# Performance work log

Measured on AMD Instinct MI355X. Metric: run time of the kernel, lower is better.

Reference implementation:

```python
import jax, jax.numpy as jnp
import numpy as np

DT = 0.01
NJ = 7
GRAV = 9.81
Q_LOWER = jnp.array([-2.9671, -1.8326, -2.9671, -3.1416, -2.9671, -0.0873, -2.9671], jnp.float32)
Q_UPPER = jnp.array([ 2.9671,  1.8326,  2.9671,  0.0,     2.9671,  3.8223,  2.9671], jnp.float32)


def _skew(v):
    z = jnp.zeros((), v.dtype)
    return jnp.stack([jnp.stack([z, -v[2], v[1]]),
                      jnp.stack([v[2], z, -v[0]]),
                      jnp.stack([-v[1], v[0], z])])


def _mot_X(E, r):
    # 6x6 spatial motion transform [[E,0],[-E*skew(r),E]]
    zero = jnp.zeros_like(E)
    top = jnp.concatenate([E, zero], axis=1)
    bot = jnp.concatenate([-E @ _skew(r), E], axis=1)
    return jnp.concatenate([top, bot], axis=0)


def _crm(v):
    # spatial motion cross-product matrix for v=[w;v0]
    Sw, Sv = _skew(v[:3]), _skew(v[3:])
    zero = jnp.zeros_like(Sw)
    top = jnp.concatenate([Sw, zero], axis=1)
    bot = jnp.concatenate([Sv, Sw], axis=1)
    return jnp.concatenate([top, bot], axis=0)


def _step_single(x, u, axes, R_tree, p_tree, I_sp):
    dt_ = x.dtype
    q = jnp.clip(x[:NJ], Q_LOWER.astype(dt_), Q_UPPER.astype(dt_))
    qd = x[NJ:]
    # forward kinematics: per-joint 6x6 child<-parent transforms and motion subspaces
    Xups, Ss = [], []
    eye3 = jnp.eye(3, dtype=dt_)
    for i in range(NJ):
        a = axes[i]
        c, s = jnp.cos(q[i]), jnp.sin(q[i])
        R = c * eye3 + s * _skew(a) + (1.0 - c) * jnp.outer(a, a)  # rodrigues
        Xj = _mot_X(R.T, jnp.zeros(3, dt_))
        Xt = _mot_X(R_tree[i], p_tree[i])
        Xups.append(Xj @ Xt)
        Ss.append(jnp.concatenate([a, jnp.zeros(3, dt_)]))
    # RNEA bias force h (qdd=0, gravity, zero base velocity, identity base pose)
    v_prev = jnp.zeros(6, dt_)
    a_prev = jnp.array([0.0, 0.0, 0.0, 0.0, 0.0, GRAV], dt_)  # a_base = -g trick
    fs = []
    for i in range(NJ):
        vJ = Ss[i] * qd[i]
        v = Xups[i] @ v_prev + vJ
        acc = Xups[i] @ a_prev + _crm(v) @ vJ
        Iv = I_sp[i] @ v
        f = I_sp[i] @ acc - _crm(v).T @ Iv  # crf(v) = -crm(v)^T
        fs.append(f)
        v_prev, a_prev = v, acc
    h = [None] * NJ
    for i in range(NJ - 1, -1, -1):
        h[i] = Ss[i] @ fs[i]
        if i > 0:
            fs[i - 1] = fs[i - 1] + Xups[i].T @ fs[i]
    h = jnp.stack(h)
    # CRBA mass matrix (serial chain, parent(i)=i-1)
    Ic = [I_sp[i] for i in range(NJ)]
    M = jnp.zeros((NJ, NJ), dt_)
    for i in range(NJ - 1, -1, -1):
        if i > 0:
            Ic[i - 1] = Ic[i - 1] + Xups[i].T @ Ic[i] @ Xups[i]
        F = Ic[i] @ Ss[i]
        M = M.at[i, i].set(Ss[i] @ F)
        for j in range(i - 1, -1, -1):
            F = Xups[j + 1].T @ F
            mij = Ss[j] @ F
            M = M.at[i, j].set(mij).at[j, i].set(mij)
    M = M + 1e-8 * jnp.eye(NJ, dtype=dt_)
    qdd = jnp.linalg.solve(M, (u - h)[:, None])[:, 0]
    qd_new = qd + DT * qdd
    q_new = q + DT * qd_new
    return jnp.concatenate([q_new, qd_new])


def setup_inputs() -> dict:
    B = 65536
    key = jax.random.key(0)
    k1, k2 = jax.random.split(key)
    x = jax.random.normal(k1, (B, 14), jnp.float32)
    u = jax.random.normal(k2, (B, 7), jnp.float32)
    rng = np.random.default_rng(0)
    # unit joint axes
    axes = rng.normal(size=(NJ, 3))
    axes = axes / np.linalg.norm(axes, axis=1, keepdims=True)
    # orthonormal fixed parent->child rotations (det +1)
    R_tree = np.empty((NJ, 3, 3))
    for i in range(NJ):
        Q, _ = np.linalg.qr(rng.normal(size=(3, 3)))
        if np.linalg.det(Q) < 0:
            Q[:, 0] = -Q[:, 0]
        R_tree[i] = Q
    p_tree = 0.2 * rng.normal(size=(NJ, 3))
    # SPD 6x6 spatial inertias: [[Ibar, m*Cx],[m*Cx^T, m*I3]]
    I_sp = np.empty((NJ, 6, 6))
    for i in range(NJ):
        m = float(rng.uniform(1.0, 5.0))
        c = 0.05 * rng.normal(size=3)
        Cx = np.array([[0, -c[2], c[1]], [c[2], 0, -c[0]], [-c[1], c[0], 0]])
        A = 0.1 * rng.normal(size=(3, 3))
        Ic_ = A @ A.T + 0.05 * np.eye(3)
        Ibar = Ic_ + m * Cx @ Cx.T
        I_sp[i] = np.block([[Ibar, m * Cx], [m * Cx.T, m * np.eye(3)]])
    return {
        "x": x, "u": u,
        "axes": jnp.asarray(axes, jnp.float32),
        "R_tree": jnp.asarray(R_tree, jnp.float32),
        "p_tree": jnp.asarray(p_tree, jnp.float32),
        "I_sp": jnp.asarray(I_sp, jnp.float32),
    }


def reference(x, u, axes, R_tree, p_tree, I_sp):
    return jax.vmap(_step_single, in_axes=(0, 0, None, None, None, None))(
        x, u, axes, R_tree, p_tree, I_sp)
```

## Files before the change

kernel.cpp:

```cpp
#include <hip/hip_runtime.h>
#include <math.h>

#define NJ 7
#define DTF 0.01f
#define GRAVF 9.81f
#define MIX(i,j) ((i)*((i)+1)/2 + (j))
#define MPAD 29
#define FSTR 43
#define SNC  15
#define QST  9

__device__ __forceinline__ void cross3(const float* a, const float* b, float* o){
    o[0] = a[1]*b[2] - a[2]*b[1];
    o[1] = a[2]*b[0] - a[0]*b[2];
    o[2] = a[0]*b[1] - a[1]*b[0];
}
__device__ __forceinline__ void mv3(const float* E, const float* x, float* y){
    y[0] = E[0]*x[0] + E[1]*x[1] + E[2]*x[2];
    y[1] = E[3]*x[0] + E[4]*x[1] + E[5]*x[2];
    y[2] = E[6]*x[0] + E[7]*x[1] + E[8]*x[2];
}
__device__ __forceinline__ void mtv3(const float* E, const float* x, float* y){
    y[0] = E[0]*x[0] + E[3]*x[1] + E[6]*x[2];
    y[1] = E[1]*x[0] + E[4]*x[1] + E[7]*x[2];
    y[2] = E[2]*x[0] + E[5]*x[1] + E[8]*x[2];
}
__device__ __forceinline__ void symv(const float* S, const float* x, float* y){
    y[0] = S[0]*x[0] + S[1]*x[1] + S[2]*x[2];
    y[1] = S[1]*x[0] + S[3]*x[1] + S[4]*x[2];
    y[2] = S[2]*x[0] + S[4]*x[1] + S[5]*x[2];
}
__device__ __forceinline__ void mm3(const float* A, const float* B, float* o){
#pragma unroll
    for (int r = 0; r < 3; r++)
#pragma unroll
        for (int c = 0; c < 3; c++)
            o[r*3+c] = A[r*3]*B[c] + A[r*3+1]*B[3+c] + A[r*3+2]*B[6+c];
}
__device__ __forceinline__ void congr(const float* E, const float* X, float* o){
    float t[9];
#pragma unroll
    for (int r = 0; r < 3; r++)
#pragma unroll
        for (int c = 0; c < 3; c++)
            t[r*3+c] = E[r]*X[c] + E[3+r]*X[3+c] + E[6+r]*X[6+c];
    mm3(t, E, o);
}
__device__ __forceinline__ void makeE(const float* a, const float* __restrict__ Rt,
                                      float s, float c, float* E){
    float omc = 1.0f - c;
    float RT[9];
    RT[0] = c + omc*a[0]*a[0];       RT[1] =  s*a[2] + omc*a[0]*a[1]; RT[2] = -s*a[1] + omc*a[0]*a[2];
    RT[3] = -s*a[2] + omc*a[1]*a[0]; RT[4] = c + omc*a[1]*a[1];       RT[5] =  s*a[0] + omc*a[1]*a[2];
    RT[6] =  s*a[1] + omc*a[2]*a[0]; RT[7] = -s*a[0] + omc*a[2]*a[1]; RT[8] = c + omc*a[2]*a[2];
    float Rl[9];
#pragma unroll
    for (int k = 0; k < 9; k++) Rl[k] = Rt[k];
    mm3(RT, Rl, E);
}
__device__ __forceinline__ void bodyI(const float* __restrict__ g_I, int i,
                                      float* SA, float* h, float& m){
    const float* I6 = g_I + i*36;
    SA[0]=I6[0]; SA[1]=I6[1]; SA[2]=I6[2];
    SA[3]=I6[7]; SA[4]=I6[8]; SA[5]=I6[14];
    h[0]=I6[16]; h[1]=I6[5]; h[2]=I6[9];
    m = I6[21];
}

__constant__ float QL_c[NJ] = {-2.9671f,-1.8326f,-2.9671f,-3.1416f,-2.9671f,-0.0873f,-2.9671f};
__constant__ float QU_c[NJ] = { 2.9671f, 1.8326f, 2.9671f, 0.0f,    2.9671f, 3.8223f, 2.9671f};

__global__ __launch_bounds__(128)
void panda_step(const float* __restrict__ x, const float* __restrict__ u,
                const float* __restrict__ g_ax, const float* __restrict__ g_Rt,
                const float* __restrict__ g_pt, const float* __restrict__ g_I,
                float* __restrict__ out, int B)
{
    __shared__ float s_M[64*MPAD];
    __shared__ float s_F[2*64*FSTR];
    __shared__ float s_snc[64*SNC];
    __shared__ float s_qd[64*QST];
    __shared__ float s_rhs[64*QST];

    const int role = threadIdx.x >> 6;
    const int lane = threadIdx.x & 63;
    const int e    = blockIdx.x*64 + lane;
    const bool act = (e < B);

    float q[NJ], qd[NJ];
    if (act && role == 0){
        float xl[14];
        const float2* x2 = (const float2*)(x + e*14);
#pragma unroll
        for (int i = 0; i < 7; i++){ float2 v = x2[i]; xl[2*i] = v.x; xl[2*i+1] = v.y; }
#pragma unroll
        for (int i = 0; i < NJ; i++){
            q[i]  = fminf(fmaxf(xl[i], QL_c[i]), QU_c[i]);
            qd[i] = xl[NJ + i];
            float s, c; __sincosf(q[i], &s, &c);
            s_snc[lane*SNC + i]     = s;
            s_snc[lane*SNC + 7 + i] = c;
            s_qd[lane*QST + i]      = qd[i];
            s_rhs[lane*QST + i]     = u[e*NJ + i];
        }
    }
    __syncthreads();

    if (act && role == 1){
        float* Fb = &s_F[64*FSTR + lane*FSTR];
        float SA[6], hc[3], mc;
        bodyI(g_I, 6, SA, hc, mc);
#pragma unroll 1
        for (int i = NJ-1; i >= 0; --i){
            float a[3] = { g_ax[3*i], g_ax[3*i+1], g_ax[3*i+2] };
            float p[3] = { g_pt[3*i], g_pt[3*i+1], g_pt[3*i+2] };
            float Ft[3]; symv(SA, a, Ft);
            Fb[i*6+0]=Ft[0]; Fb[i*6+1]=Ft[1]; Fb[i*6+2]=Ft[2];
            Fb[i*6+3] = a[1]*hc[2] - a[2]*hc[1];
            Fb[i*6+4] = a[2]*hc[0] - a[0]*hc[2];
            Fb[i*6+5] = a[0]*hc[1] - a[1]*hc[0];
#pragma unroll 1
            for (int k = i; k < NJ; ++k){
                float f0=Fb[k*6], f1=Fb[k*6+1], f2=Fb[k*6+2];
                s_M[lane*MPAD + k*(k+1)/2 + i] = a[0]*f0 + a[1]*f1 + a[2]*f2;
            }
            if (i > 0){
                float snv = s_snc[lane*SNC+i], csv = s_snc[lane*SNC+7+i];
                float E[9]; makeE(a, g_Rt + 9*i, snv, csv, E);
                float SAm[6], hm[3], mm_;
                bodyI(g_I, i-1, SAm, hm, mm_);
                float Af[9] = {SA[0],SA[1],SA[2], SA[1],SA[3],SA[4], SA[2],SA[4],SA[5]};
                float Ap[9]; congr(E, Af, Ap);
                float hr[3]; mtv3(E, hc, hr);
                float hpd = hr[0]*p[0]+hr[1]*p[1]+hr[2]*p[2];
                float ppd = p[0]*p[0]+p[1]*p[1]+p[2]*p[2];
                float dga = 2.0f*hpd + mc*ppd;
                SA[0] = Ap[0] - 2.0f*p[0]*hr[0] - mc*p[0]*p[0] + dga + SAm[0];
                SA[1] = Ap[1] - p[0]*hr[1] - hr[0]*p[1] - mc*p[0]*p[1] + SAm[1];
                SA[2] = Ap[2] - p[0]*hr[2] - hr[0]*p[2] - mc*p[0]*p[2] + SAm[2];
                SA[3] = Ap[4] - 2.0f*p[1]*hr[1] - mc*p[1]*p[1] + dga + SAm[3];
                SA[4] = Ap[5] - p[1]*hr[2] - hr[1]*p[2] - mc*p[1]*p[2] + SAm[4];
                SA[5] = Ap[8] - 2.0f*p[2]*hr[2] - mc*p[2]*p[2] + dga + SAm[5];
                hc[0] = hr[0] + mc*p[0] + hm[0];
                hc[1] = hr[1] + mc*p[1] + hm[1];
                hc[2] = hr[2] + mc*p[2] + hm[2];
                mc += mm_;
#pragma unroll 1
                for (int k = i; k < NJ; ++k){
                    float ft[3] = {Fb[k*6+0], Fb[k*6+1], Fb[k*6+2]};
                    float fb[3] = {Fb[k*6+3], Fb[k*6+4], Fb[k*6+5]};
                    float tm[3], tf[3], cp[3];
                    mtv3(E, ft, tm); mtv3(E, fb, tf);
                    cross3(p, tf, cp);
                    Fb[k*6+0]=tm[0]+cp[0]; Fb[k*6+1]=tm[1]+cp[1]; Fb[k*6+2]=tm[2]+cp[2];
                    Fb[k*6+3]=tf[0];       Fb[k*6+4]=tf[1];       Fb[k*6+5]=tf[2];
                }
            }
        }
        float Mx[28];
#pragma unroll
        for (int j = 0; j < 28; j++) Mx[j] = s_M[lane*MPAD + j];
#pragma unroll
        for (int i = 0; i < NJ; i++) Mx[MIX(i,i)] += 1e-8f;
#pragma unroll
        for (int k = 0; k < NJ; k++){
            float d = Mx[MIX(k,k)];
#pragma unroll
            for (int j = 0; j < NJ; j++) if (j < k) d -= Mx[MIX(k,j)]*Mx[MIX(k,j)];
            float linv = __builtin_amdgcn_rsqf(d);
            Mx[MIX(k,k)] = linv;
#pragma unroll
            for (int i2 = k+1; i2 < NJ; i2++){
                float s2 = Mx[MIX(i2,k)];
#pragma unroll
                for (int j = 0; j < NJ; j++) if (j < k) s2 -= Mx[MIX(i2,j)]*Mx[MIX(k,j)];
                Mx[MIX(i2,k)] = s2 * linv;
            }
        }
#pragma unroll
        for (int j = 0; j < 28; j++) s_M[lane*MPAD + j] = Mx[j];
    }
    else if (act){
        float* Fb = &s_F[lane*FSTR];
        float w[3]  = {0.f,0.f,0.f}, vl[3] = {0.f,0.f,0.f};
        float aw[3] = {0.f,0.f,0.f}, av[3] = {0.f,0.f,GRAVF};
#pragma unroll 1
        for (int i = 0; i < NJ; ++i){
            float a[3] = { g_ax[3*i], g_ax[3*i+1], g_ax[3*i+2] };
            float p[3] = { g_pt[3*i], g_pt[3*i+1], g_pt[3*i+2] };
            float snv = s_snc[lane*SNC+i], csv = s_snc[lane*SNC+7+i];
            float qdi = s_qd[lane*QST+i];
            float E[9]; makeE(a, g_Rt + 9*i, snv, csv, E);
            float tw[3]; mv3(E, w, tw);
            float nw[3] = { tw[0]+a[0]*qdi, tw[1]+a[1]*qdi, tw[2]+a[2]*qdi };
            float cwp[3]; cross3(w, p, cwp);
            float t1[3] = { vl[0]+cwp[0], vl[1]+cwp[1], vl[2]+cwp[2] };
            float nvl[3]; mv3(E, t1, nvl);
            float taw[3]; mv3(E, aw, taw);
            float cna[3]; cross3(nw, a, cna);
            float naw[3] = { taw[0]+qdi*cna[0], taw[1]+qdi*cna[1], taw[2]+qdi*cna[2] };
            float cap[3]; cross3(aw, p, cap);
            float t2[3] = { av[0]+cap[0], av[1]+cap[1], av[2]+cap[2] };
            float tav[3]; mv3(E, t2, tav);
            float cva[3]; cross3(nvl, a, cva);
            float nav[3] = { tav[0]+qdi*cva[0], tav[1]+qdi*cva[1], tav[2]+qdi*cva[2] };
            float SAi[6], hi[3], mi; bodyI(g_I, i, SAi, hi, mi);
            float Ivt[3], Iat[3], hxv[3], hxa[3];
            symv(SAi, nw, Ivt);  cross3(hi, nvl, hxv);
            symv(SAi, naw, Iat); cross3(hi, nav, hxa);
#pragma unroll
            for (int k = 0; k < 3; k++){ Ivt[k] += hxv[k]; Iat[k] += hxa[k]; }
            float hxw[3], hxaw[3];
            cross3(hi, nw, hxw); cross3(hi, naw, hxaw);
            float Ivb[3] = { mi*nvl[0]-hxw[0], mi*nvl[1]-hxw[1], mi*nvl[2]-hxw[2] };
            float Iab[3] = { mi*nav[0]-hxaw[0], mi*nav[1]-hxaw[1], mi*nav[2]-hxaw[2] };
            float c1[3], c2[3], c3[3];
            cross3(nw, Ivt, c1); cross3(nvl, Ivb, c2); cross3(nw, Ivb, c3);
            Fb[i*6+0] = Iat[0]+c1[0]+c2[0];
            Fb[i*6+1] = Iat[1]+c1[1]+c2[1];
            Fb[i*6+2] = Iat[2]+c1[2]+c2[2];
            Fb[i*6+3] = Iab[0]+c3[0];
            Fb[i*6+4] = Iab[1]+c3[1];
            Fb[i*6+5] = Iab[2]+c3[2];
#pragma unroll
            for (int k = 0; k < 3; k++){ w[k]=nw[k]; vl[k]=nvl[k]; aw[k]=naw[k]; av[k]=nav[k]; }
        }
#pragma unroll 1
        for (int i = NJ-1; i >= 0; --i){
            float a[3] = { g_ax[3*i], g_ax[3*i+1], g_ax[3*i+2] };
            float f0=Fb[i*6+0], f1=Fb[i*6+1], f2=Fb[i*6+2];
            s_rhs[lane*QST+i] -= a[0]*f0 + a[1]*f1 + a[2]*f2;
            if (i > 0){
                float p[3] = { g_pt[3*i], g_pt[3*i+1], g_pt[3*i+2] };
                float snv = s_snc[lane*SNC+i], csv = s_snc[lane*SNC+7+i];
                float E[9]; makeE(a, g_Rt + 9*i, snv, csv, E);
                float ftop[3] = {f0, f1, f2};
                float fbot[3] = {Fb[i*6+3], Fb[i*6+4], Fb[i*6+5]};
                float tm[3], tf[3], cp[3];
                mtv3(E, ftop, tm); mtv3(E, fbot, tf);
                cross3(p, tf, cp);
                Fb[(i-1)*6+0] += tm[0]+cp[0];
                Fb[(i-1)*6+1] += tm[1]+cp[1];
                Fb[(i-1)*6+2] += tm[2]+cp[2];
                Fb[(i-1)*6+3] += tf[0];
                Fb[(i-1)*6+4] += tf[1];
                Fb[(i-1)*6+5] += tf[2];
            }
        }
    }

    __syncthreads();

    if (act && role == 0){
        float Mx[28];
#pragma unroll
        for (int j = 0; j < 28; j++) Mx[j] = s_M[lane*MPAD + j];
        float rhs[NJ];
#pragma unroll
        for (int i = 0; i < NJ; i++) rhs[i] = s_rhs[lane*QST + i];
        float y[NJ];
#pragma unroll
        for (int i = 0; i < NJ; i++){
            float s2 = rhs[i];
#pragma unroll
            for (int j = 0; j < NJ; j++) if (j < i) s2 -= Mx[MIX(i,j)]*y[j];
            y[i] = s2 * Mx[MIX(i,i)];
        }
        float z[NJ];
#pragma unroll
        for (int i = NJ-1; i >= 0; i--){
            float s2 = y[i];
#pragma unroll
            for (int j = NJ-1; j >= 0; j--) if (j > i) s2 -= Mx[MIX(j,i)]*z[j];
            z[i] = s2 * Mx[MIX(i,i)];
        }
        float o14[14];
#pragma unroll
        for (int i = 0; i < NJ; i++){
            float qdn = qd[i] + DTF*z[i];
            o14[i]      = q[i] + DTF*qdn;
            o14[NJ + i] = qdn;
        }
        float2* o2 = (float2*)(out + e*14);
#pragma unroll
        for (int i = 0; i < 7; i++){ float2 v; v.x = o14[2*i]; v.y = o14[2*i+1]; o2[i] = v; }
    }
}

extern "C" void kernel_launch(void* const* d_in, const int* in_sizes, int n_in,
                              void* d_out, int out_size, void* d_ws, size_t ws_size,
                              hipStream_t stream) {
    const float* x   = (const float*)d_in[0];
    const float* u   = (const float*)d_in[1];
    const float* ax  = (const float*)d_in[2];
    const float* Rt  = (const float*)d_in[3];
    const float* pt  = (const float*)d_in[4];
    const float* Isp = (const float*)d_in[5];
    float* out = (float*)d_out;
    int B = in_sizes[0] / 14;
    int grid = (B + 63) / 64;
    hipLaunchKernelGGL(panda_step, dim3(grid), dim3(128), 0, stream,
                       x, u, ax, Rt, pt, Isp, out, B);
}
```

Baseline: 77.28 us.

## Drop prologue barrier by loading inputs per role and move Cholesky to solver

Each wavefront role now loads x and computes its own sin/cos in private shared buffers, which removes the first __syncthreads and the serial prologue that only role 0 ran. The Cholesky factorization moves from the mass-matrix wavefront into the final solve section after the barrier, which shortens the longer CRBA branch. In exchange the sincos work and the x loads are done twice, once by each wavefront.

```diff
diff --git a/kernel.cpp b/kernel.cpp
--- a/kernel.cpp
+++ b/kernel.cpp
@@ -7,8 +7,8 @@
 #define MIX(i,j) ((i)*((i)+1)/2 + (j))
 #define MPAD 29
 #define FSTR 43
-#define SNC  15
-#define QST  9
+#define P0S  29
+#define P1S  15
 
 __device__ __forceinline__ void cross3(const float* a, const float* b, float* o){
     o[0] = a[1]*b[2] - a[2]*b[1];
@@ -78,9 +78,8 @@
 {
     __shared__ float s_M[64*MPAD];
     __shared__ float s_F[2*64*FSTR];
-    __shared__ float s_snc[64*SNC];
-    __shared__ float s_qd[64*QST];
-    __shared__ float s_rhs[64*QST];
+    __shared__ float s_p0[64*P0S];
+    __shared__ float s_p1[64*P1S];
 
     const int role = threadIdx.x >> 6;
     const int lane = threadIdx.x & 63;
@@ -88,25 +87,21 @@
     const bool act = (e < B);
 
     float q[NJ], qd[NJ];
-    if (act && role == 0){
-        float xl[14];
-        const float2* x2 = (const float2*)(x + e*14);
-#pragma unroll
-        for (int i = 0; i < 7; i++){ float2 v = x2[i]; xl[2*i] = v.x; xl[2*i+1] = v.y; }
-#pragma unroll
-        for (int i = 0; i < NJ; i++){
-            q[i]  = fminf(fmaxf(xl[i], QL_c[i]), QU_c[i]);
-            qd[i] = xl[NJ + i];
-            float s, c; __sincosf(q[i], &s, &c);
-            s_snc[lane*SNC + i]     = s;
-            s_snc[lane*SNC + 7 + i] = c;
-            s_qd[lane*QST + i]      = qd[i];
-            s_rhs[lane*QST + i]     = u[e*NJ + i];
-        }
-    }
-    __syncthreads();
 
     if (act && role == 1){
+        {
+            const float2* x2 = (const float2*)(x + e*14);
+            float q8[8];
+#pragma unroll
+            for (int i = 0; i < 4; i++){ float2 v = x2[i]; q8[2*i] = v.x; q8[2*i+1] = v.y; }
+#pragma unroll
+            for (int i = 0; i < NJ; i++){
+                float qi = fminf(fmaxf(q8[i], QL_c[i]), QU_c[i]);
+                float s, c; __sincosf(qi, &s, &c);
+                s_p1[lane*P1S + i]     = s;
+                s_p1[lane*P1S + 7 + i] = c;
+            }
+        }
         float* Fb = &s_F[64*FSTR + lane*FSTR];
         float SA[6], hc[3], mc;
         bodyI(g_I, 6, SA, hc, mc);
@@ -125,7 +120,7 @@
                 s_M[lane*MPAD + k*(k+1)/2 + i] = a[0]*f0 + a[1]*f1 + a[2]*f2;
             }
             if (i > 0){
-                float snv = s_snc[lane*SNC+i], csv = s_snc[lane*SNC+7+i];
+                float snv = s_p1[lane*P1S+i], csv = s_p1[lane*P1S+7+i];
                 float E[9]; makeE(a, g_Rt + 9*i, snv, csv, E);
                 float SAm[6], hm[3], mm_;
                 bodyI(g_I, i-1, SAm, hm, mm_);
@@ -157,30 +152,24 @@
                 }
             }
         }
-        float Mx[28];
-#pragma unroll
-        for (int j = 0; j < 28; j++) Mx[j] = s_M[lane*MPAD + j];
-#pragma unroll
-        for (int i = 0; i < NJ; i++) Mx[MIX(i,i)] += 1e-8f;
-#pragma unroll
-        for (int k = 0; k < NJ; k++){
-            float d = Mx[MIX(k,k)];
-#pragma unroll
-            for (int j = 0; j < NJ; j++) if (j < k) d -= Mx[MIX(k,j)]*Mx[MIX(k,j)];
-            float linv = __builtin_amdgcn_rsqf(d);
-            Mx[MIX(k,k)] = linv;
-#pragma unroll
-            for (int i2 = k+1; i2 < NJ; i2++){
-                float s2 = Mx[MIX(i2,k)];
-#pragma unroll
-                for (int j = 0; j < NJ; j++) if (j < k) s2 -= Mx[MIX(i2,j)]*Mx[MIX(k,j)];
-                Mx[MIX(i2,k)] = s2 * linv;
-            }
-        }
-#pragma unroll
-        for (int j = 0; j < 28; j++) s_M[lane*MPAD + j] = Mx[j];
     }
     else if (act){
+        {
+            float xl[14];
+            const float2* x2 = (const float2*)(x + e*14);
+#pragma unroll
+            for (int i = 0; i < 7; i++){ float2 v = x2[i]; xl[2*i] = v.x; xl[2*i+1] = v.y; }
+#pragma unroll
+            for (int i = 0; i < NJ; i++){
+                q[i]  = fminf(fmaxf(xl[i], QL_c[i]), QU_c[i]);
+                qd[i] = xl[NJ + i];
+                float s, c; __sincosf(q[i], &s, &c);
+                s_p0[lane*P0S + i]      = s;
+                s_p0[lane*P0S + 7 + i]  = c;
+                s_p0[lane*P0S + 14 + i] = qd[i];
+                s_p0[lane*P0S + 21 + i] = u[e*NJ + i];
+            }
+        }
         float* Fb = &s_F[lane*FSTR];
         float w[3]  = {0.f,0.f,0.f}, vl[3] = {0.f,0.f,0.f};
         float aw[3] = {0.f,0.f,0.f}, av[3] = {0.f,0.f,GRAVF};
@@ -188,8 +177,8 @@
         for (int i = 0; i < NJ; ++i){
             float a[3] = { g_ax[3*i], g_ax[3*i+1], g_ax[3*i+2] };
             float p[3] = { g_pt[3*i], g_pt[3*i+1], g_pt[3*i+2] };
-            float snv = s_snc[lane*SNC+i], csv = s_snc[lane*SNC+7+i];
-            float qdi = s_qd[lane*QST+i];
+            float snv = s_p0[lane*P0S+i], csv = s_p0[lane*P0S+7+i];
+            float qdi = s_p0[lane*P0S+14+i];
             float E[9]; makeE(a, g_Rt + 9*i, snv, csv, E);
             float tw[3]; mv3(E, w, tw);
             float nw[3] = { tw[0]+a[0]*qdi, tw[1]+a[1]*qdi, tw[2]+a[2]*qdi };
@@ -229,10 +218,10 @@
         for (int i = NJ-1; i >= 0; --i){
             float a[3] = { g_ax[3*i], g_ax[3*i+1], g_ax[3*i+2] };
             float f0=Fb[i*6+0], f1=Fb[i*6+1], f2=Fb[i*6+2];
-            s_rhs[lane*QST+i] -= a[0]*f0 + a[1]*f1 + a[2]*f2;
+            s_p0[lane*P0S+21+i] -= a[0]*f0 + a[1]*f1 + a[2]*f2;
             if (i > 0){
                 float p[3] = { g_pt[3*i], g_pt[3*i+1], g_pt[3*i+2] };
-                float snv = s_snc[lane*SNC+i], csv = s_snc[lane*SNC+7+i];
+                float snv = s_p0[lane*P0S+i], csv = s_p0[lane*P0S+7+i];
                 float E[9]; makeE(a, g_Rt + 9*i, snv, csv, E);
                 float ftop[3] = {f0, f1, f2};
                 float fbot[3] = {Fb[i*6+3], Fb[i*6+4], Fb[i*6+5]};
@@ -255,9 +244,26 @@
         float Mx[28];
 #pragma unroll
         for (int j = 0; j < 28; j++) Mx[j] = s_M[lane*MPAD + j];
+#pragma unroll
+        for (int i = 0; i < NJ; i++) Mx[MIX(i,i)] += 1e-8f;
+#pragma unroll
+        for (int k = 0; k < NJ; k++){
+            float d = Mx[MIX(k,k)];
+#pragma unroll
+            for (int j = 0; j < NJ; j++) if (j < k) d -= Mx[MIX(k,j)]*Mx[MIX(k,j)];
+            float linv = __builtin_amdgcn_rsqf(d);
+            Mx[MIX(k,k)] = linv;
+#pragma unroll
+            for (int i2 = k+1; i2 < NJ; i2++){
+                float s2 = Mx[MIX(i2,k)];
+#pragma unroll
+                for (int j = 0; j < NJ; j++) if (j < k) s2 -= Mx[MIX(i2,j)]*Mx[MIX(k,j)];
+                Mx[MIX(i2,k)] = s2 * linv;
+            }
+        }
         float rhs[NJ];
 #pragma unroll
-        for (int i = 0; i < NJ; i++) rhs[i] = s_rhs[lane*QST + i];
+        for (int i = 0; i < NJ; i++) rhs[i] = s_p0[lane*P0S + 21 + i];
         float y[NJ];
 #pragma unroll
         for (int i = 0; i < NJ; i++){
```

After: 77.62 us. About the same (+0.4%).
